# Optimization experiments

Hardware: AMD Instinct MI355X
Metric: run time of the kernel (lower is better)

## Reference

```python
import jax, jax.numpy as jnp
import numpy as np

B, S, I, H, O, L = 64, 256, 512, 1024, 512, 2


def _lin(key, out_d, in_d, scale=0.03):
    return jax.random.normal(key, (out_d, in_d), dtype=jnp.float32) * scale


def setup_inputs() -> dict:
    key = jax.random.key(0)
    ks = jax.random.split(key, 32)
    inp = {"x": jax.random.normal(ks[0], (B, S, I), dtype=jnp.float32)}
    k = 1
    for li, in_d in enumerate([I, H]):
        for g in ["z", "r", "g"]:
            inp[f"Wx{g}{li}"] = _lin(ks[k], H, in_d); k += 1
            inp[f"bx{g}{li}"] = jnp.zeros((H,), jnp.float32)
            inp[f"Wh{g}{li}"] = _lin(ks[k], H, H); k += 1
    inp["Why"] = _lin(ks[k], O, H); k += 1
    inp["bhy"] = jnp.zeros((O,), jnp.float32)
    return inp


def _gru_layer(xs, Wxz, bxz, Whz, Wxr, bxr, Whr, Wxg, bxg, Whg):
    # xs: (B, S, D_in). Precompute all input projections as one big GEMM each.
    xz = jnp.einsum('bsi,hi->sbh', xs, Wxz) + bxz  # (S,B,H)
    xr = jnp.einsum('bsi,hi->sbh', xs, Wxr) + bxr
    xg = jnp.einsum('bsi,hi->sbh', xs, Wxg) + bxg
    h0 = jnp.zeros((xs.shape[0], Whz.shape[0]), xs.dtype)

    def step(h, t):
        xzt, xrt, xgt = t
        z = jax.nn.sigmoid(xzt + h @ Whz.T)
        r = jax.nn.sigmoid(xrt + h @ Whr.T)
        g = jnp.tanh(xgt + (r * h) @ Whg.T)
        h_new = z * h + (1.0 - z) * g
        return h_new, h_new

    h_last, hs = jax.lax.scan(step, h0, (xz, xr, xg))
    return jnp.transpose(hs, (1, 0, 2)), h_last  # (B,S,H), (B,H)


def reference(x, Wxz0, bxz0, Whz0, Wxr0, bxr0, Whr0, Wxg0, bxg0, Whg0,
              Wxz1, bxz1, Whz1, Wxr1, bxr1, Whr1, Wxg1, bxg1, Whg1,
              Why, bhy):
    y0, h0 = _gru_layer(x, Wxz0, bxz0, Whz0, Wxr0, bxr0, Whr0, Wxg0, bxg0, Whg0)
    y1, h1 = _gru_layer(y0, Wxz1, bxz1, Whz1, Wxr1, bxr1, Whr1, Wxg1, bxg1, Whg1)
    layer_output = jnp.einsum('bsh,oh->bso', y1, Why) + bhy  # (B,S,O)
    hidden_state = jnp.stack([h0, h1], axis=1)  # (B,L,H)
    return layer_output, hidden_state
```

## Files before the change

### kernel.cpp

```cpp
#include <hip/hip_runtime.h>
#include <hip/hip_bf16.h>

#define B 64
#define SEQ 256
#define IN 512
#define HD 1024
#define ODIM 512
#define WGTH 512

typedef __attribute__((ext_vector_type(8))) short bf16x8;
typedef __attribute__((ext_vector_type(4))) float f32x4;
typedef __attribute__((ext_vector_type(4))) unsigned short u16x4;

__device__ __forceinline__ f32x4 mfma16(bf16x8 a, bf16x8 b, f32x4 c) {
  return __builtin_amdgcn_mfma_f32_16x16x32_bf16(a, b, c, 0, 0, 0);
}

__device__ __forceinline__ unsigned short f2bf(float f) {
  unsigned u = __builtin_bit_cast(unsigned, f);
  u += 0x7FFFu + ((u >> 16) & 1u);
  return (unsigned short)(u >> 16);
}

__device__ __forceinline__ float sigmoidf_(float x) { return 1.f / (1.f + expf(-x)); }

__device__ __forceinline__ void stc16(unsigned short* p, bf16x8 v) {
  asm volatile("global_store_dwordx4 %0, %1, off sc1" : : "v"(p), "v"(v) : "memory");
}

__device__ __forceinline__ void ldg16(bf16x8& d, const unsigned short* p) {
  asm volatile("global_load_dwordx4 %0, %1, off sc0 sc1" : "=v"(d) : "v"(p) : "memory");
}

template <int N>
__device__ __forceinline__ void vmwait() {
  asm volatile("s_waitcnt vmcnt(%0)" :: "i"(N) : "memory");
  __builtin_amdgcn_sched_barrier(0);
}

__device__ __forceinline__ void flag_set(unsigned* fl, int wgl, unsigned val) {
  if (threadIdx.x == 0) {
    unsigned* p = fl + wgl * 16;
    asm volatile("s_waitcnt vmcnt(0)\n\t"
                 "global_store_dword %0, %1, off sc0 sc1"
                 :: "v"(p), "v"(val) : "memory");
  }
}

__device__ __forceinline__ void flag_poll(const unsigned* fl, unsigned tgt) {
  if (threadIdx.x < 64) {
    const unsigned* p = fl + threadIdx.x * 16;
    for (;;) {
      unsigned v;
      asm volatile("global_load_dword %0, %1, off sc0 sc1\n\t"
                   "s_waitcnt vmcnt(0)" : "=v"(v) : "v"(p) : "memory");
      if (__ballot(v < tgt) == 0ull) break;
      __builtin_amdgcn_s_sleep(2);
    }
  }
  __syncthreads();
}

__device__ __forceinline__ void flag_poll2(const unsigned* f1, unsigned t1,
                                           const unsigned* f2, unsigned t2) {
  if (threadIdx.x < 64) {
    const unsigned* p1 = f1 + threadIdx.x * 16;
    const unsigned* p2 = f2 + threadIdx.x * 16;
    for (;;) {
      unsigned v1, v2;
      asm volatile("global_load_dword %0, %2, off sc0 sc1\n\t"
                   "global_load_dword %1, %3, off sc0 sc1\n\t"
                   "s_waitcnt vmcnt(0)"
                   : "=v"(v1), "=v"(v2) : "v"(p1), "v"(p2) : "memory");
      if ((__ballot(v1 < t1) | __ballot(v2 < t2)) == 0ull) break;
      __builtin_amdgcn_s_sleep(2);
    }
  }
  __syncthreads();
}

__global__ void f32_to_bf16_k(const float* __restrict__ s, unsigned short* __restrict__ d, int n) {
  int i = (blockIdx.x * blockDim.x + threadIdx.x) * 4;
  if (i < n) {
    float4 v = *reinterpret_cast<const float4*>(s + i);
    u16x4 o;
    o.x = f2bf(v.x); o.y = f2bf(v.y); o.z = f2bf(v.z); o.w = f2bf(v.w);
    *reinterpret_cast<u16x4*>(d + i) = o;
  }
}

struct PackSeg { const float* s; unsigned short* d; int N; int K; };
struct PackP { PackSeg seg[13]; };

__global__ void pack_w(PackP P) {
  PackSeg sg = P.seg[blockIdx.y];
  const int kc_n = sg.K >> 5;
  const int total = (sg.N * sg.K) >> 3;
  for (int i = blockIdx.x * blockDim.x + threadIdx.x; i < total; i += gridDim.x * blockDim.x) {
    int lane = i & 63;
    int block = i >> 6;
    int kc = block % kc_n;
    int nt = block / kc_n;
    int n = nt * 16 + (lane & 15);
    int k = kc * 32 + (lane >> 4) * 8;
    const float* s = sg.s + (size_t)n * sg.K + k;
    float4 v0 = *(const float4*)(s);
    float4 v1 = *(const float4*)(s + 4);
    u16x4 o0, o1;
    o0.x = f2bf(v0.x); o0.y = f2bf(v0.y); o0.z = f2bf(v0.z); o0.w = f2bf(v0.w);
    o1.x = f2bf(v1.x); o1.y = f2bf(v1.y); o1.z = f2bf(v1.z); o1.w = f2bf(v1.w);
    unsigned short* dp = sg.d + (size_t)i * 8;
    *(u16x4*)(dp) = o0;
    *(u16x4*)(dp + 4) = o1;
  }
}

struct GruP {
  const unsigned short* xbf;
  const unsigned short* wx[2][3];
  const unsigned short* wh[2][3];
  const float* bx[2][3];
  unsigned short* h0b[4];
  unsigned short* h1b;
  unsigned short* rh[2];
  unsigned short* y1;
  float* outh;
  unsigned* bar;
};

#define GISS(mt, sArr, baseP) do { \
    const unsigned short* _p = (baseP) + (size_t)(16 * (mt) + lo) * HD; \
    ldg16(sArr[0], _p);      ldg16(sArr[1], _p + 32); \
    ldg16(sArr[2], _p + 64); ldg16(sArr[3], _p + 96); \
  } while (0)

#define GCMP2(mt, sArr, wz_, wr_) do { \
    f32x4 _a = vz[mt], _b = vr[mt]; \
    _a = mfma16(sArr[0], wz_[0], _a); _b = mfma16(sArr[0], wr_[0], _b); \
    _a = mfma16(sArr[1], wz_[1], _a); _b = mfma16(sArr[1], wr_[1], _b); \
    _a = mfma16(sArr[2], wz_[2], _a); _b = mfma16(sArr[2], wr_[2], _b); \
    _a = mfma16(sArr[3], wz_[3], _a); _b = mfma16(sArr[3], wr_[3], _b); \
    vz[mt] = _a; vr[mt] = _b; \
  } while (0)

#define YCMP3(mt, s) do { \
    f32x4 _z = vz[mt], _r = vr[mt], _g = vg[mt]; \
    _z = mfma16(s[0], wxz[0], _z); _r = mfma16(s[0], wxr[0], _r); _g = mfma16(s[0], wxg[0], _g); \
    _z = mfma16(s[1], wxz[1], _z); _r = mfma16(s[1], wxr[1], _r); _g = mfma16(s[1], wxg[1], _g); \
    _z = mfma16(s[2], wxz[2], _z); _r = mfma16(s[2], wxr[2], _r); _g = mfma16(s[2], wxg[2], _g); \
    _z = mfma16(s[3], wxz[3], _z); _r = mfma16(s[3], wxr[3], _r); _g = mfma16(s[3], wxg[3], _g); \
    vz[mt] = _z; vr[mt] = _r; vg[mt] = _g; \
  } while (0)

#define RCMP1(mt, s) do { \
    f32x4 _a = vg[mt]; \
    _a = mfma16(s[0], whg[0], _a); _a = mfma16(s[1], whg[1], _a); \
    _a = mfma16(s[2], whg[2], _a); _a = mfma16(s[3], whg[3], _a); \
    vg[mt] = _a; \
  } while (0)

template <int LAYER>
__device__ void gru_body(const GruP& P, f32x4 (*red)[7][64]) {
  const int wgl = (int)blockIdx.x & 63;
  const int tid = threadIdx.x;
  const int w = tid >> 6;
  const int lane = tid & 63;
  const int lo = lane & 15, hi = lane >> 4;
  const int cC = wgl * 16 + lo;
  constexpr int KX = LAYER ? HD : IN;
  constexpr int CX = KX / 256;
  constexpr int CH = 4;
  const int kslH = w * 128 + hi * 8;
  const int kslX = w * (KX >> 3) + hi * 8;

  bf16x8 whz[CH], whr[CH], whg[CH], wxz[CX], wxr[CX], wxg[CX];
  #pragma unroll
  for (int c = 0; c < CH; ++c) {
    size_t o = ((size_t)wgl * (HD / 32) + w * CH + c) * 512 + (size_t)lane * 8;
    whz[c] = *(const bf16x8*)(P.wh[LAYER][0] + o);
    whr[c] = *(const bf16x8*)(P.wh[LAYER][1] + o);
    whg[c] = *(const bf16x8*)(P.wh[LAYER][2] + o);
  }
  #pragma unroll
  for (int c = 0; c < CX; ++c) {
    size_t o = ((size_t)wgl * (KX / 32) + w * CX + c) * 512 + (size_t)lane * 8;
    wxz[c] = *(const bf16x8*)(P.wx[LAYER][0] + o);
    wxr[c] = *(const bf16x8*)(P.wx[LAYER][1] + o);
    wxg[c] = *(const bf16x8*)(P.wx[LAYER][2] + o);
  }
  const float bz = P.bx[LAYER][0][cC];
  const float br = P.bx[LAYER][1][cC];
  const float bg = P.bx[LAYER][2][cC];
  unsigned short* RH = P.rh[LAYER];

  unsigned* flAmy = P.bar + (LAYER * 2 + 0) * 1024;
  unsigned* flBmy = P.bar + (LAYER * 2 + 1) * 1024;
  unsigned* flBot = P.bar + ((1 - LAYER) * 2 + 1) * 1024;

  f32x4 hreg = {0.f, 0.f, 0.f, 0.f};
  f32x4 zreg = {0.f, 0.f, 0.f, 0.f};

  for (int t = 0; t < SEQ; ++t) {
    f32x4 vz[4], vr[4], vg[4];
    bf16x8 sS0[4], sS1[4];

    if constexpr (!LAYER) {
      const unsigned short* xB = P.xbf + (size_t)t * IN + kslX;
      #pragma unroll
      for (int mt = 0; mt < 4; ++mt) {
        const unsigned short* xp = xB + (size_t)(16 * mt + lo) * (SEQ * IN);
        bf16x8 x0 = *(const bf16x8*)(xp);
        bf16x8 x1 = *(const bf16x8*)(xp + 32);
        f32x4 a = {0,0,0,0}, b = {0,0,0,0}, c = {0,0,0,0};
        a = mfma16(x0, wxz[0], a); a = mfma16(x1, wxz[1], a);
        b = mfma16(x0, wxr[0], b); b = mfma16(x1, wxr[1], b);
        c = mfma16(x0, wxg[0], c); c = mfma16(x1, wxg[1], c);
        vz[mt] = a; vr[mt] = b; vg[mt] = c;
      }
      if (t) flag_poll(flBmy, (unsigned)t);
    } else {
      flag_poll2(flBot, (unsigned)(t + 1), flBmy, (unsigned)t);
    }

    if constexpr (LAYER) {
      const unsigned short* yB = P.h0b[t & 3] + kslH;
      #pragma unroll
      for (int mt = 0; mt < 4; ++mt) { vz[mt] = {0,0,0,0}; vr[mt] = {0,0,0,0}; vg[mt] = {0,0,0,0}; }
      GISS(0, sS0, yB); GISS(1, sS1, yB);
      vmwait<4>(); YCMP3(0, sS0); GISS(2, sS0, yB);
      vmwait<4>(); YCMP3(1, sS1); GISS(3, sS1, yB);
      vmwait<4>(); YCMP3(2, sS0);
      vmwait<0>(); YCMP3(3, sS1);
    }
    {
      const unsigned short* hB = (LAYER ? P.h1b : P.h0b[(t + 3) & 3]) + kslH;
      GISS(0, sS0, hB); GISS(1, sS1, hB);
      vmwait<4>(); GCMP2(0, sS0, whz, whr); GISS(2, sS0, hB);
      vmwait<4>(); GCMP2(1, sS1, whz, whr); GISS(3, sS1, hB);
      vmwait<4>(); GCMP2(2, sS0, whz, whr);
      vmwait<0>(); GCMP2(3, sS1, whz, whr);
    }
    f32x4 keepz, keepr;
    #pragma unroll
    for (int mt = 0; mt < 4; ++mt) {
      if (w == mt) { keepz = vz[mt]; keepr = vr[mt]; }
      else {
        int col = (w > mt) ? (w - 1) : w;
        red[mt][col][lane] = vz[mt];
        red[4 + mt][col][lane] = vr[mt];
      }
    }
    __syncthreads();
    if (w < 4) {
      f32x4 sz = keepz, sr = keepr;
      #pragma unroll
      for (int j = 0; j < 7; ++j) { sz += red[w][j][lane]; sr += red[4 + w][j][lane]; }
      unsigned short* tl = (unsigned short*)&red[4 + w][0][0];
      #pragma unroll
      for (int q = 0; q < 4; ++q) {
        float z = sigmoidf_(sz[q] + bz);
        float r = sigmoidf_(sr[q] + br);
        zreg[q] = z;
        tl[(4 * hi + q) * 24 + lo] = f2bf(r * hreg[q]);
      }
      asm volatile("s_waitcnt lgkmcnt(0)" ::: "memory");
      __builtin_amdgcn_sched_barrier(0);
      if (lane < 32) {
        const int r8 = lane >> 1, s8 = (lane & 1) * 8;
        bf16x8 v = *(const bf16x8*)(tl + r8 * 24 + s8);
        stc16(RH + (size_t)(16 * w + r8) * HD + wgl * 16 + s8, v);
      }
    }
    asm volatile("s_waitcnt vmcnt(0)" ::: "memory");
    __syncthreads();
    flag_set(flAmy, wgl, (unsigned)(t + 1));

    if constexpr (!LAYER) {
      if (t >= 4) flag_poll2(flAmy, (unsigned)(t + 1), flBot, (unsigned)(t - 3));
      else        flag_poll(flAmy, (unsigned)(t + 1));
    } else {
      flag_poll(flAmy, (unsigned)(t + 1));
    }

    {
      const unsigned short* rB = RH + kslH;
      GISS(0, sS0, rB); GISS(1, sS1, rB);
      vmwait<4>(); RCMP1(0, sS0); GISS(2, sS0, rB);
      vmwait<4>(); RCMP1(1, sS1); GISS(3, sS1, rB);
      vmwait<4>(); RCMP1(2, sS0);
      vmwait<0>(); RCMP1(3, sS1);
    }
    f32x4 keepg;
    #pragma unroll
    for (int mt = 0; mt < 4; ++mt) {
      if (w == mt) keepg = vg[mt];
      else { int col = (w > mt) ? (w - 1) : w; red[mt][col][lane] = vg[mt]; }
    }
    __syncthreads();
    if (w < 4) {
      f32x4 sg = keepg;
      #pragma unroll
      for (int j = 0; j < 7; ++j) sg += red[w][j][lane];
      unsigned short* hW = LAYER ? P.h1b : P.h0b[t & 3];
      unsigned short* tl = (unsigned short*)&red[4 + w][0][0];
      #pragma unroll
      for (int q = 0; q < 4; ++q) {
        const int row = 16 * w + 4 * hi + q;
        float g = tanhf(sg[q] + bg);
        float hn = zreg[q] * hreg[q] + (1.f - zreg[q]) * g;
        hreg[q] = hn;
        tl[(4 * hi + q) * 24 + lo] = f2bf(hn);
        if (t == SEQ - 1) P.outh[(size_t)row * (2 * HD) + LAYER * HD + cC] = hn;
      }
      asm volatile("s_waitcnt lgkmcnt(0)" ::: "memory");
      __builtin_amdgcn_sched_barrier(0);
      if (lane < 32) {
        const int r8 = lane >> 1, s8 = (lane & 1) * 8;
        bf16x8 v = *(const bf16x8*)(tl + r8 * 24 + s8);
        stc16(hW + (size_t)(16 * w + r8) * HD + wgl * 16 + s8, v);
        if (LAYER) {
          unsigned short* yp = P.y1 + ((size_t)(16 * w + r8) * SEQ + t) * HD + wgl * 16 + s8;
          *(bf16x8*)yp = v;
        }
      }
    }
    asm volatile("s_waitcnt vmcnt(0)" ::: "memory");
    __syncthreads();
    flag_set(flBmy, wgl, (unsigned)(t + 1));
  }
}

__global__ __launch_bounds__(WGTH, 1) void gru_persist(GruP P) {
  __shared__ f32x4 red[8][7][64];
  if (blockIdx.x < 64) gru_body<0>(P, red);
  else gru_body<1>(P, red);
}

__global__ __launch_bounds__(256) void out_gemm(const unsigned short* __restrict__ Y,
                                                const unsigned short* __restrict__ Wp,
                                                const float* __restrict__ bias,
                                                float* __restrict__ C) {
  const int w = threadIdx.x >> 6, lane = threadIdx.x & 63;
  const int lo = lane & 15, hi = lane >> 4;
  const int row0 = blockIdx.x * 64;
  const int col0 = blockIdx.y * 64 + w * 16;
  const unsigned short* wp = Wp + ((size_t)(col0 >> 4) * (HD >> 5)) * 512 + (size_t)lane * 8;
  const unsigned short* yp = Y + (size_t)(row0 + lo) * HD + hi * 8;
  f32x4 a0 = {0,0,0,0}, a1 = {0,0,0,0}, a2 = {0,0,0,0}, a3 = {0,0,0,0};
  #pragma unroll 4
  for (int kb = 0; kb < (HD >> 5); ++kb) {
    bf16x8 bw = *(const bf16x8*)(wp + kb * 512);
    const int k = kb * 32;
    a0 = mfma16(*(const bf16x8*)(yp + k), bw, a0);
    a1 = mfma16(*(const bf16x8*)(yp + (size_t)16 * HD + k), bw, a1);
    a2 = mfma16(*(const bf16x8*)(yp + (size_t)32 * HD + k), bw, a2);
    a3 = mfma16(*(const bf16x8*)(yp + (size_t)48 * HD + k), bw, a3);
  }
  const int cc = col0 + lo;
  const float bb = bias[cc];
  const int rbase = row0 + 4 * hi;
  #pragma unroll
  for (int q = 0; q < 4; ++q) {
    C[(size_t)(rbase + q) * ODIM + cc]      = a0[q] + bb;
    C[(size_t)(rbase + 16 + q) * ODIM + cc] = a1[q] + bb;
    C[(size_t)(rbase + 32 + q) * ODIM + cc] = a2[q] + bb;
    C[(size_t)(rbase + 48 + q) * ODIM + cc] = a3[q] + bb;
  }
}

extern "C" void kernel_launch(void* const* d_in, const int* in_sizes, int n_in,
                              void* d_out, int out_size, void* d_ws, size_t ws_size,
                              hipStream_t stream) {
  char* ws = (char*)d_ws;
  size_t off = 0;
  auto take = [&](size_t bytes) -> char* {
    char* p = ws + off;
    off += (bytes + 255) & ~(size_t)255;
    return p;
  };

  unsigned short* xbf = (unsigned short*)take((size_t)B * SEQ * IN * 2);
  unsigned short *wx0[3], *wh0[3], *wx1[3], *wh1[3];
  for (int g = 0; g < 3; ++g) wx0[g] = (unsigned short*)take((size_t)HD * IN * 2);
  for (int g = 0; g < 3; ++g) wh0[g] = (unsigned short*)take((size_t)HD * HD * 2);
  for (int g = 0; g < 3; ++g) wx1[g] = (unsigned short*)take((size_t)HD * HD * 2);
  for (int g = 0; g < 3; ++g) wh1[g] = (unsigned short*)take((size_t)HD * HD * 2);
  unsigned short* whyb = (unsigned short*)take((size_t)ODIM * HD * 2);
  unsigned short* y1 = (unsigned short*)take((size_t)B * SEQ * HD * 2);
  char* state0 = ws + off;
  unsigned short* h0r[4];
  for (int i = 0; i < 4; ++i) h0r[i] = (unsigned short*)take((size_t)B * HD * 2);
  unsigned short* h1b = (unsigned short*)take((size_t)B * HD * 2);
  unsigned short* rh0 = (unsigned short*)take((size_t)B * HD * 2);
  unsigned short* rh1 = (unsigned short*)take((size_t)B * HD * 2);
  unsigned* bar = (unsigned*)take((size_t)4 * 4096);
  size_t stateBytes = (size_t)((ws + off) - state0);

  {
    int n = B * SEQ * IN;
    hipLaunchKernelGGL(f32_to_bf16_k, dim3((n / 4 + 255) / 256), dim3(256), 0, stream,
                       (const float*)d_in[0], xbf, n);
  }

  {
    PackP pp;
    int s = 0;
    pp.seg[s++] = { (const float*)d_in[1],  wx0[0], HD, IN };
    pp.seg[s++] = { (const float*)d_in[4],  wx0[1], HD, IN };
    pp.seg[s++] = { (const float*)d_in[7],  wx0[2], HD, IN };
    pp.seg[s++] = { (const float*)d_in[3],  wh0[0], HD, HD };
    pp.seg[s++] = { (const float*)d_in[6],  wh0[1], HD, HD };
    pp.seg[s++] = { (const float*)d_in[9],  wh0[2], HD, HD };
    pp.seg[s++] = { (const float*)d_in[10], wx1[0], HD, HD };
    pp.seg[s++] = { (const float*)d_in[13], wx1[1], HD, HD };
    pp.seg[s++] = { (const float*)d_in[16], wx1[2], HD, HD };
    pp.seg[s++] = { (const float*)d_in[12], wh1[0], HD, HD };
    pp.seg[s++] = { (const float*)d_in[15], wh1[1], HD, HD };
    pp.seg[s++] = { (const float*)d_in[18], wh1[2], HD, HD };
    pp.seg[s++] = { (const float*)d_in[19], whyb, ODIM, HD };
    hipLaunchKernelGGL(pack_w, dim3(512, 13), dim3(256), 0, stream, pp);
  }

  hipMemsetAsync(state0, 0, stateBytes, stream);

  GruP P;
  P.xbf = xbf;
  for (int g = 0; g < 3; ++g) {
    P.wx[0][g] = wx0[g]; P.wh[0][g] = wh0[g];
    P.wx[1][g] = wx1[g]; P.wh[1][g] = wh1[g];
  }
  P.bx[0][0] = (const float*)d_in[2];  P.bx[0][1] = (const float*)d_in[5];  P.bx[0][2] = (const float*)d_in[8];
  P.bx[1][0] = (const float*)d_in[11]; P.bx[1][1] = (const float*)d_in[14]; P.bx[1][2] = (const float*)d_in[17];
  for (int i = 0; i < 4; ++i) P.h0b[i] = h0r[i];
  P.h1b = h1b;
  P.rh[0] = rh0; P.rh[1] = rh1;
  P.y1 = y1;
  P.outh = (float*)d_out + (size_t)B * SEQ * ODIM;
  P.bar = bar;

  hipLaunchKernelGGL(gru_persist, dim3(128), dim3(WGTH), 0, stream, P);

  hipLaunchKernelGGL(out_gemm, dim3((B * SEQ) / 64, ODIM / 64), dim3(256), 0, stream,
                     (const unsigned short*)y1, (const unsigned short*)whyb,
                     (const float*)d_in[20], (float*)d_out);
}
```

Before: 4.924 ms.

## Double-buffer h1 and r*h buffers and switch to per-wave flag polling

Adds double-buffered h1 and r*h staging buffers so producers can write the next step without waiting for every workgroup to finish reading the current one. The WG-wide barrier polls are relaxed to check the previous step's flags. Each wave now polls only the 8 flags of the workgroups whose rows it consumes, so waves can proceed independently without a __syncthreads. This is meant to shorten the critical-path synchronization latency per timestep in the persistent GRU. It adds more subtle cross-step ordering that could introduce races if the lagged polls are insufficient.

```diff
diff --git a/kernel.cpp b/kernel.cpp
--- a/kernel.cpp
+++ b/kernel.cpp
@@ -61,22 +61,34 @@
   __syncthreads();
 }
 
-__device__ __forceinline__ void flag_poll2(const unsigned* f1, unsigned t1,
-                                           const unsigned* f2, unsigned t2) {
-  if (threadIdx.x < 64) {
-    const unsigned* p1 = f1 + threadIdx.x * 16;
-    const unsigned* p2 = f2 + threadIdx.x * 16;
-    for (;;) {
-      unsigned v1, v2;
+__device__ __forceinline__ void wpoll1(const unsigned* fl, int w, unsigned tgt) {
+  const int lane = threadIdx.x & 63;
+  const unsigned* p = fl + (size_t)((w << 3) + (lane & 7)) * 16;
+  for (;;) {
+    unsigned v = tgt;
+    if (lane < 8)
+      asm volatile("global_load_dword %0, %1, off sc0 sc1\n\t"
+                   "s_waitcnt vmcnt(0)" : "=v"(v) : "v"(p) : "memory");
+    if (__ballot(v < tgt) == 0ull) break;
+    __builtin_amdgcn_s_sleep(1);
+  }
+}
+
+__device__ __forceinline__ void wpoll2w(const unsigned* f1, unsigned t1,
+                                        const unsigned* f2, unsigned t2, int w) {
+  const int lane = threadIdx.x & 63;
+  const unsigned* p1 = f1 + (size_t)((w << 3) + (lane & 7)) * 16;
+  const unsigned* p2 = f2 + (size_t)((w << 3) + (lane & 7)) * 16;
+  for (;;) {
+    unsigned v1 = t1, v2 = t2;
+    if (lane < 8)
       asm volatile("global_load_dword %0, %2, off sc0 sc1\n\t"
                    "global_load_dword %1, %3, off sc0 sc1\n\t"
                    "s_waitcnt vmcnt(0)"
                    : "=v"(v1), "=v"(v2) : "v"(p1), "v"(p2) : "memory");
-      if ((__ballot(v1 < t1) | __ballot(v2 < t2)) == 0ull) break;
-      __builtin_amdgcn_s_sleep(2);
-    }
-  }
-  __syncthreads();
+    if ((__ballot(v1 < t1) | __ballot(v2 < t2)) == 0ull) break;
+    __builtin_amdgcn_s_sleep(1);
+  }
 }
 
 __global__ void f32_to_bf16_k(const float* __restrict__ s, unsigned short* __restrict__ d, int n) {
@@ -121,8 +133,8 @@
   const unsigned short* wh[2][3];
   const float* bx[2][3];
   unsigned short* h0b[4];
-  unsigned short* h1b;
-  unsigned short* rh[2];
+  unsigned short* h1b[2];
+  unsigned short* rh[2][2];
   unsigned short* y1;
   float* outh;
   unsigned* bar;
@@ -191,7 +203,6 @@
   const float bz = P.bx[LAYER][0][cC];
   const float br = P.bx[LAYER][1][cC];
   const float bg = P.bx[LAYER][2][cC];
-  unsigned short* RH = P.rh[LAYER];
 
   unsigned* flAmy = P.bar + (LAYER * 2 + 0) * 1024;
   unsigned* flBmy = P.bar + (LAYER * 2 + 1) * 1024;
@@ -203,6 +214,7 @@
   for (int t = 0; t < SEQ; ++t) {
     f32x4 vz[4], vr[4], vg[4];
     bf16x8 sS0[4], sS1[4];
+    unsigned short* RHcur = P.rh[LAYER][t & 1];
 
     if constexpr (!LAYER) {
       const unsigned short* xB = P.xbf + (size_t)t * IN + kslX;
@@ -217,9 +229,12 @@
         c = mfma16(x0, wxg[0], c); c = mfma16(x1, wxg[1], c);
         vz[mt] = a; vr[mt] = b; vg[mt] = c;
       }
-      if (t) flag_poll(flBmy, (unsigned)t);
+      if (t >= 2) flag_poll(flBmy, (unsigned)(t - 1));
+      if (t) wpoll1(flBmy, w, (unsigned)t);
     } else {
-      flag_poll2(flBot, (unsigned)(t + 1), flBmy, (unsigned)t);
+      if (t >= 2) flag_poll(flBmy, (unsigned)(t - 1));
+      if (t) wpoll2w(flBot, (unsigned)(t + 1), flBmy, (unsigned)t, w);
+      else   wpoll1(flBot, w, (unsigned)(t + 1));
     }
 
     if constexpr (LAYER) {
@@ -233,7 +248,7 @@
       vmwait<0>(); YCMP3(3, sS1);
     }
     {
-      const unsigned short* hB = (LAYER ? P.h1b : P.h0b[(t + 3) & 3]) + kslH;
+      const unsigned short* hB = (LAYER ? P.h1b[(t + 1) & 1] : P.h0b[(t + 3) & 3]) + kslH;
       GISS(0, sS0, hB); GISS(1, sS1, hB);
       vmwait<4>(); GCMP2(0, sS0, whz, whr); GISS(2, sS0, hB);
       vmwait<4>(); GCMP2(1, sS1, whz, whr); GISS(3, sS1, hB);
@@ -268,22 +283,21 @@
       if (lane < 32) {
         const int r8 = lane >> 1, s8 = (lane & 1) * 8;
         bf16x8 v = *(const bf16x8*)(tl + r8 * 24 + s8);
-        stc16(RH + (size_t)(16 * w + r8) * HD + wgl * 16 + s8, v);
+        stc16(RHcur + (size_t)(16 * w + r8) * HD + wgl * 16 + s8, v);
       }
     }
     asm volatile("s_waitcnt vmcnt(0)" ::: "memory");
     __syncthreads();
     flag_set(flAmy, wgl, (unsigned)(t + 1));
 
+    if (t) flag_poll(flAmy, (unsigned)t);
     if constexpr (!LAYER) {
-      if (t >= 4) flag_poll2(flAmy, (unsigned)(t + 1), flBot, (unsigned)(t - 3));
-      else        flag_poll(flAmy, (unsigned)(t + 1));
-    } else {
-      flag_poll(flAmy, (unsigned)(t + 1));
-    }
+      if (t >= 4) flag_poll(flBot, (unsigned)(t - 3));
+    }
+    wpoll1(flAmy, w, (unsigned)(t + 1));
 
     {
-      const unsigned short* rB = RH + kslH;
+      const unsigned short* rB = RHcur + kslH;
       GISS(0, sS0, rB); GISS(1, sS1, rB);
       vmwait<4>(); RCMP1(0, sS0); GISS(2, sS0, rB);
       vmwait<4>(); RCMP1(1, sS1); GISS(3, sS1, rB);
@@ -301,7 +315,7 @@
       f32x4 sg = keepg;
       #pragma unroll
       for (int j = 0; j < 7; ++j) sg += red[w][j][lane];
-      unsigned short* hW = LAYER ? P.h1b : P.h0b[t & 3];
+      unsigned short* hW = LAYER ? P.h1b[t & 1] : P.h0b[t & 3];
       unsigned short* tl = (unsigned short*)&red[4 + w][0][0];
       #pragma unroll
       for (int q = 0; q < 4; ++q) {
@@ -390,9 +404,11 @@
   char* state0 = ws + off;
   unsigned short* h0r[4];
   for (int i = 0; i < 4; ++i) h0r[i] = (unsigned short*)take((size_t)B * HD * 2);
-  unsigned short* h1b = (unsigned short*)take((size_t)B * HD * 2);
-  unsigned short* rh0 = (unsigned short*)take((size_t)B * HD * 2);
-  unsigned short* rh1 = (unsigned short*)take((size_t)B * HD * 2);
+  unsigned short* h1p[2];
+  for (int i = 0; i < 2; ++i) h1p[i] = (unsigned short*)take((size_t)B * HD * 2);
+  unsigned short* rhp[2][2];
+  for (int l = 0; l < 2; ++l)
+    for (int i = 0; i < 2; ++i) rhp[l][i] = (unsigned short*)take((size_t)B * HD * 2);
   unsigned* bar = (unsigned*)take((size_t)4 * 4096);
   size_t stateBytes = (size_t)((ws + off) - state0);
 
@@ -432,8 +448,9 @@
   P.bx[0][0] = (const float*)d_in[2];  P.bx[0][1] = (const float*)d_in[5];  P.bx[0][2] = (const float*)d_in[8];
   P.bx[1][0] = (const float*)d_in[11]; P.bx[1][1] = (const float*)d_in[14]; P.bx[1][2] = (const float*)d_in[17];
   for (int i = 0; i < 4; ++i) P.h0b[i] = h0r[i];
-  P.h1b = h1b;
-  P.rh[0] = rh0; P.rh[1] = rh1;
+  for (int i = 0; i < 2; ++i) P.h1b[i] = h1p[i];
+  for (int l = 0; l < 2; ++l)
+    for (int i = 0; i < 2; ++i) P.rh[l][i] = rhp[l][i];
   P.y1 = y1;
   P.outh = (float*)d_out + (size_t)B * SEQ * ODIM;
   P.bar = bar;
```

Measured after the change: 4.218 ms. 14.3% less time.

## Replace flag barriers with NaN-sentinel data polling on ring-buffered hidden states

Applied to the files above, without the earlier changes.

Hidden-state and r*h buffers become multi-slot rings pre-filled with a bf16 NaN sentinel. Consumers spin on the data itself until no sentinel remains, and producers re-poison a slot a few steps ahead, so most flag polls between workgroups go away. The aim is to cut per-step cross-workgroup synchronisation latency in the persistent GRU kernel. The cost is larger loads that are fully waited on instead of pipelined, and correctness now depends on no real value ever matching the sentinel bit pattern and on stores being visible in order.

```diff
diff --git a/kernel.cpp b/kernel.cpp
--- a/kernel.cpp
+++ b/kernel.cpp
@@ -11,6 +11,7 @@
 typedef __attribute__((ext_vector_type(8))) short bf16x8;
 typedef __attribute__((ext_vector_type(4))) float f32x4;
 typedef __attribute__((ext_vector_type(4))) unsigned short u16x4;
+typedef __attribute__((ext_vector_type(4))) unsigned int u32x4;
 
 __device__ __forceinline__ f32x4 mfma16(bf16x8 a, bf16x8 b, f32x4 c) {
   return __builtin_amdgcn_mfma_f32_16x16x32_bf16(a, b, c, 0, 0, 0);
@@ -36,6 +37,24 @@
 __device__ __forceinline__ void vmwait() {
   asm volatile("s_waitcnt vmcnt(%0)" :: "i"(N) : "memory");
   __builtin_amdgcn_sched_barrier(0);
+}
+
+__device__ __forceinline__ bf16x8 sent8() {
+  bf16x8 v;
+  #pragma unroll
+  for (int i = 0; i < 8; ++i) v[i] = (short)0x7FC0;
+  return v;
+}
+
+__device__ __forceinline__ unsigned badchk(bf16x8 v) {
+  u32x4 u = __builtin_bit_cast(u32x4, v);
+  unsigned b = 0;
+  #pragma unroll
+  for (int i = 0; i < 4; ++i) {
+    unsigned x = u[i] ^ 0x7FC07FC0u;
+    b |= (x - 0x00010001u) & ~x & 0x80008000u;
+  }
+  return b;
 }
 
 __device__ __forceinline__ void flag_set(unsigned* fl, int wgl, unsigned val) {
@@ -61,24 +80,6 @@
   __syncthreads();
 }
 
-__device__ __forceinline__ void flag_poll2(const unsigned* f1, unsigned t1,
-                                           const unsigned* f2, unsigned t2) {
-  if (threadIdx.x < 64) {
-    const unsigned* p1 = f1 + threadIdx.x * 16;
-    const unsigned* p2 = f2 + threadIdx.x * 16;
-    for (;;) {
-      unsigned v1, v2;
-      asm volatile("global_load_dword %0, %2, off sc0 sc1\n\t"
-                   "global_load_dword %1, %3, off sc0 sc1\n\t"
-                   "s_waitcnt vmcnt(0)"
-                   : "=v"(v1), "=v"(v2) : "v"(p1), "v"(p2) : "memory");
-      if ((__ballot(v1 < t1) | __ballot(v2 < t2)) == 0ull) break;
-      __builtin_amdgcn_s_sleep(2);
-    }
-  }
-  __syncthreads();
-}
-
 __global__ void f32_to_bf16_k(const float* __restrict__ s, unsigned short* __restrict__ d, int n) {
   int i = (blockIdx.x * blockDim.x + threadIdx.x) * 4;
   if (i < n) {
@@ -87,6 +88,12 @@
     o.x = f2bf(v.x); o.y = f2bf(v.y); o.z = f2bf(v.z); o.w = f2bf(v.w);
     *reinterpret_cast<u16x4*>(d + i) = o;
   }
+}
+
+__global__ void fill_sent(unsigned* __restrict__ d, size_t n) {
+  size_t i = (size_t)blockIdx.x * blockDim.x + threadIdx.x;
+  size_t st = (size_t)gridDim.x * blockDim.x;
+  for (; i < n; i += st) d[i] = 0x7FC07FC0u;
 }
 
 struct PackSeg { const float* s; unsigned short* d; int N; int K; };
@@ -120,9 +127,9 @@
   const unsigned short* wx[2][3];
   const unsigned short* wh[2][3];
   const float* bx[2][3];
-  unsigned short* h0b[4];
-  unsigned short* h1b;
-  unsigned short* rh[2];
+  unsigned short* h0r;
+  unsigned short* h1r;
+  unsigned short* rhr[2];
   unsigned short* y1;
   float* outh;
   unsigned* bar;
@@ -132,6 +139,19 @@
     const unsigned short* _p = (baseP) + (size_t)(16 * (mt) + lo) * HD; \
     ldg16(sArr[0], _p);      ldg16(sArr[1], _p + 32); \
     ldg16(sArr[2], _p + 64); ldg16(sArr[3], _p + 96); \
+  } while (0)
+
+#define SPOLL(baseP) do { \
+    for (;;) { \
+      GISS(0, s0, baseP); GISS(1, s1, baseP); GISS(2, s2, baseP); GISS(3, s3, baseP); \
+      vmwait<0>(); \
+      unsigned _bad = badchk(s0[0]) | badchk(s0[1]) | badchk(s0[2]) | badchk(s0[3]) \
+                    | badchk(s1[0]) | badchk(s1[1]) | badchk(s1[2]) | badchk(s1[3]) \
+                    | badchk(s2[0]) | badchk(s2[1]) | badchk(s2[2]) | badchk(s2[3]) \
+                    | badchk(s3[0]) | badchk(s3[1]) | badchk(s3[2]) | badchk(s3[3]); \
+      if (__ballot(_bad != 0) == 0ull) break; \
+      __builtin_amdgcn_s_sleep(1); \
+    } \
   } while (0)
 
 #define GCMP2(mt, sArr, wz_, wr_) do { \
@@ -172,6 +192,7 @@
   constexpr int CH = 4;
   const int kslH = w * 128 + hi * 8;
   const int kslX = w * (KX >> 3) + hi * 8;
+  const size_t SLOT = (size_t)B * HD;
 
   bf16x8 whz[CH], whr[CH], whg[CH], wxz[CX], wxr[CX], wxg[CX];
   #pragma unroll
@@ -191,18 +212,19 @@
   const float bz = P.bx[LAYER][0][cC];
   const float br = P.bx[LAYER][1][cC];
   const float bg = P.bx[LAYER][2][cC];
-  unsigned short* RH = P.rh[LAYER];
+  unsigned short* RHr = P.rhr[LAYER];
 
   unsigned* flAmy = P.bar + (LAYER * 2 + 0) * 1024;
   unsigned* flBmy = P.bar + (LAYER * 2 + 1) * 1024;
   unsigned* flBot = P.bar + ((1 - LAYER) * 2 + 1) * 1024;
 
+  const bf16x8 SENT = sent8();
   f32x4 hreg = {0.f, 0.f, 0.f, 0.f};
   f32x4 zreg = {0.f, 0.f, 0.f, 0.f};
 
   for (int t = 0; t < SEQ; ++t) {
     f32x4 vz[4], vr[4], vg[4];
-    bf16x8 sS0[4], sS1[4];
+    bf16x8 s0[4], s1[4], s2[4], s3[4];
 
     if constexpr (!LAYER) {
       const unsigned short* xB = P.xbf + (size_t)t * IN + kslX;
@@ -217,29 +239,32 @@
         c = mfma16(x0, wxg[0], c); c = mfma16(x1, wxg[1], c);
         vz[mt] = a; vr[mt] = b; vg[mt] = c;
       }
-      if (t) flag_poll(flBmy, (unsigned)t);
     } else {
-      flag_poll2(flBot, (unsigned)(t + 1), flBmy, (unsigned)t);
-    }
+      #pragma unroll
+      for (int mt = 0; mt < 4; ++mt) { vz[mt] = {0,0,0,0}; vr[mt] = {0,0,0,0}; vg[mt] = {0,0,0,0}; }
+    }
+
+    if (t >= 2) flag_poll(flBmy, (unsigned)(t - 1));
 
     if constexpr (LAYER) {
-      const unsigned short* yB = P.h0b[t & 3] + kslH;
-      #pragma unroll
-      for (int mt = 0; mt < 4; ++mt) { vz[mt] = {0,0,0,0}; vr[mt] = {0,0,0,0}; vg[mt] = {0,0,0,0}; }
-      GISS(0, sS0, yB); GISS(1, sS1, yB);
-      vmwait<4>(); YCMP3(0, sS0); GISS(2, sS0, yB);
-      vmwait<4>(); YCMP3(1, sS1); GISS(3, sS1, yB);
-      vmwait<4>(); YCMP3(2, sS0);
-      vmwait<0>(); YCMP3(3, sS1);
-    }
-    {
-      const unsigned short* hB = (LAYER ? P.h1b : P.h0b[(t + 3) & 3]) + kslH;
-      GISS(0, sS0, hB); GISS(1, sS1, hB);
-      vmwait<4>(); GCMP2(0, sS0, whz, whr); GISS(2, sS0, hB);
-      vmwait<4>(); GCMP2(1, sS1, whz, whr); GISS(3, sS1, hB);
-      vmwait<4>(); GCMP2(2, sS0, whz, whr);
-      vmwait<0>(); GCMP2(3, sS1, whz, whr);
-    }
+      const unsigned short* yB = P.h0r + (size_t)(t & 7) * SLOT + kslH;
+      SPOLL(yB);
+      YCMP3(0, s0); YCMP3(1, s1); YCMP3(2, s2); YCMP3(3, s3);
+      if (t) {
+        const unsigned short* hB = P.h1r + (size_t)((t - 1) & 3) * SLOT + kslH;
+        SPOLL(hB);
+        GCMP2(0, s0, whz, whr); GCMP2(1, s1, whz, whr);
+        GCMP2(2, s2, whz, whr); GCMP2(3, s3, whz, whr);
+      }
+    } else {
+      if (t) {
+        const unsigned short* hB = P.h0r + (size_t)((t - 1) & 7) * SLOT + kslH;
+        SPOLL(hB);
+        GCMP2(0, s0, whz, whr); GCMP2(1, s1, whz, whr);
+        GCMP2(2, s2, whz, whr); GCMP2(3, s3, whz, whr);
+      }
+    }
+
     f32x4 keepz, keepr;
     #pragma unroll
     for (int mt = 0; mt < 4; ++mt) {
@@ -267,28 +292,25 @@
       __builtin_amdgcn_sched_barrier(0);
       if (lane < 32) {
         const int r8 = lane >> 1, s8 = (lane & 1) * 8;
+        const size_t off = (size_t)(16 * w + r8) * HD + wgl * 16 + s8;
         bf16x8 v = *(const bf16x8*)(tl + r8 * 24 + s8);
-        stc16(RH + (size_t)(16 * w + r8) * HD + wgl * 16 + s8, v);
+        stc16(RHr + (size_t)(t & 3) * SLOT + off, v);
+        stc16(RHr + (size_t)((t + 2) & 3) * SLOT + off, SENT);
       }
     }
     asm volatile("s_waitcnt vmcnt(0)" ::: "memory");
     __syncthreads();
     flag_set(flAmy, wgl, (unsigned)(t + 1));
 
+    if (t) flag_poll(flAmy, (unsigned)t);
     if constexpr (!LAYER) {
-      if (t >= 4) flag_poll2(flAmy, (unsigned)(t + 1), flBot, (unsigned)(t - 3));
-      else        flag_poll(flAmy, (unsigned)(t + 1));
-    } else {
-      flag_poll(flAmy, (unsigned)(t + 1));
+      if (t >= 4) flag_poll(flBot, (unsigned)(t - 3));
     }
 
     {
-      const unsigned short* rB = RH + kslH;
-      GISS(0, sS0, rB); GISS(1, sS1, rB);
-      vmwait<4>(); RCMP1(0, sS0); GISS(2, sS0, rB);
-      vmwait<4>(); RCMP1(1, sS1); GISS(3, sS1, rB);
-      vmwait<4>(); RCMP1(2, sS0);
-      vmwait<0>(); RCMP1(3, sS1);
+      const unsigned short* rB = RHr + (size_t)(t & 3) * SLOT + kslH;
+      SPOLL(rB);
+      RCMP1(0, s0); RCMP1(1, s1); RCMP1(2, s2); RCMP1(3, s3);
     }
     f32x4 keepg;
     #pragma unroll
@@ -301,7 +323,6 @@
       f32x4 sg = keepg;
       #pragma unroll
       for (int j = 0; j < 7; ++j) sg += red[w][j][lane];
-      unsigned short* hW = LAYER ? P.h1b : P.h0b[t & 3];
       unsigned short* tl = (unsigned short*)&red[4 + w][0][0];
       #pragma unroll
       for (int q = 0; q < 4; ++q) {
@@ -316,11 +337,16 @@
       __builtin_amdgcn_sched_barrier(0);
       if (lane < 32) {
         const int r8 = lane >> 1, s8 = (lane & 1) * 8;
+        const size_t off = (size_t)(16 * w + r8) * HD + wgl * 16 + s8;
         bf16x8 v = *(const bf16x8*)(tl + r8 * 24 + s8);
-        stc16(hW + (size_t)(16 * w + r8) * HD + wgl * 16 + s8, v);
-        if (LAYER) {
+        if constexpr (LAYER) {
+          stc16(P.h1r + (size_t)(t & 3) * SLOT + off, v);
+          stc16(P.h1r + (size_t)((t + 2) & 3) * SLOT + off, SENT);
           unsigned short* yp = P.y1 + ((size_t)(16 * w + r8) * SEQ + t) * HD + wgl * 16 + s8;
           *(bf16x8*)yp = v;
+        } else {
+          stc16(P.h0r + (size_t)(t & 7) * SLOT + off, v);
+          stc16(P.h0r + (size_t)((t + 4) & 7) * SLOT + off, SENT);
         }
       }
     }
@@ -387,14 +413,13 @@
   for (int g = 0; g < 3; ++g) wh1[g] = (unsigned short*)take((size_t)HD * HD * 2);
   unsigned short* whyb = (unsigned short*)take((size_t)ODIM * HD * 2);
   unsigned short* y1 = (unsigned short*)take((size_t)B * SEQ * HD * 2);
-  char* state0 = ws + off;
-  unsigned short* h0r[4];
-  for (int i = 0; i < 4; ++i) h0r[i] = (unsigned short*)take((size_t)B * HD * 2);
-  unsigned short* h1b = (unsigned short*)take((size_t)B * HD * 2);
-  unsigned short* rh0 = (unsigned short*)take((size_t)B * HD * 2);
-  unsigned short* rh1 = (unsigned short*)take((size_t)B * HD * 2);
+  const size_t SLOTB = (size_t)B * HD * 2;
+  unsigned short* rings = (unsigned short*)take(20 * SLOTB);
+  unsigned short* h0r  = rings;
+  unsigned short* h1r  = rings + 8 * (SLOTB / 2);
+  unsigned short* rh0r = rings + 12 * (SLOTB / 2);
+  unsigned short* rh1r = rings + 16 * (SLOTB / 2);
   unsigned* bar = (unsigned*)take((size_t)4 * 4096);
-  size_t stateBytes = (size_t)((ws + off) - state0);
 
   {
     int n = B * SEQ * IN;
@@ -421,7 +446,9 @@
     hipLaunchKernelGGL(pack_w, dim3(512, 13), dim3(256), 0, stream, pp);
   }
 
-  hipMemsetAsync(state0, 0, stateBytes, stream);
+  hipLaunchKernelGGL(fill_sent, dim3(2048), dim3(256), 0, stream,
+                     (unsigned*)rings, 20 * SLOTB / 4);
+  hipMemsetAsync(bar, 0, (size_t)4 * 4096, stream);
 
   GruP P;
   P.xbf = xbf;
@@ -431,9 +458,10 @@
   }
   P.bx[0][0] = (const float*)d_in[2];  P.bx[0][1] = (const float*)d_in[5];  P.bx[0][2] = (const float*)d_in[8];
   P.bx[1][0] = (const float*)d_in[11]; P.bx[1][1] = (const float*)d_in[14]; P.bx[1][2] = (const float*)d_in[17];
-  for (int i = 0; i < 4; ++i) P.h0b[i] = h0r[i];
-  P.h1b = h1b;
-  P.rh[0] = rh0; P.rh[1] = rh1;
+  P.h0r = h0r;
+  P.h1r = h1r;
+  P.rhr[0] = rh0r;
+  P.rhr[1] = rh1r;
   P.y1 = y1;
   P.outh = (float*)d_out + (size_t)B * SEQ * ODIM;
   P.bar = bar;
```

Result: slower. 6.412 ms (+30.2%).
